# Performance work log

Measured on AMD Instinct MI355X. Metric: run time of the kernel, lower is better.

Reference implementation:

```python
import jax, jax.numpy as jnp
import numpy as np
from jax import lax

B, PN, NS = 8, 16384, 256
KDIM, HID = 512, 384
HALF = HID // 2
EPS = 1e-5


def setup_inputs() -> dict:
    key = jax.random.key(0)
    ks = jax.random.split(key, 12)
    s = lambda fan: np.float32(1.0 / np.sqrt(fan))
    inp = {
        "p": jax.random.normal(ks[0], (B, PN, 3), jnp.float32),
        "N": NS,
        "patch_feature": jax.random.normal(ks[1], (B, KDIM, 1), jnp.float32),
        # Linear(k_dim, hidden)
        "W_feat": jax.random.normal(ks[2], (KDIM, HID), jnp.float32) * s(KDIM),
        "b_feat": jax.random.normal(ks[3], (HID,), jnp.float32) * s(KDIM),
        # Linear(3, hidden//2)
        "W_coord": jax.random.normal(ks[4], (3, HALF), jnp.float32) * s(3),
        "b_coord": jax.random.normal(ks[5], (HALF,), jnp.float32) * s(3),
        # Conv1d(hidden+hidden//2, hidden, 1) == per-point linear, weight (out,in)
        "W1": jax.random.normal(ks[6], (HID, HID + HALF), jnp.float32) * s(HID + HALF),
        "b1": jax.random.normal(ks[7], (HID,), jnp.float32) * s(HID + HALF),
        "g1": jnp.ones((HID,), jnp.float32),
        "be1": jnp.zeros((HID,), jnp.float32),
        # Conv1d(hidden, hidden, 1)
        "W2": jax.random.normal(ks[8], (HID, HID), jnp.float32) * s(HID),
        "b2": jax.random.normal(ks[9], (HID,), jnp.float32) * s(HID),
        "g2": jnp.ones((HID,), jnp.float32),
        "be2": jnp.zeros((HID,), jnp.float32),
    }
    return inp


def farthest_point_sample(points, k):
    """points: (B, N, C) -> (B, k, C). Deterministic start index 0 per batch."""
    b, n, c = points.shape

    def step(carry, _):
        dist, far = carry
        centroid = jnp.take_along_axis(points, far[:, None, None], axis=1)  # (B,1,C)
        d = jnp.sum((points - centroid) ** 2, axis=-1)                      # (B,N)
        dist = jnp.minimum(dist, d)
        new_far = jnp.argmax(dist, axis=-1)
        return (dist, new_far), far

    init = (jnp.full((b, n), 1e10, points.dtype), jnp.zeros((b,), jnp.int32))
    _, idx = lax.scan(step, init, None, length=k)  # idx: (k, B)
    idx = idx.T                                    # (B, k)
    return jnp.take_along_axis(points, idx[:, :, None], axis=1)  # (B,k,C)


def batchnorm(x, gamma, beta):
    """x: (B, L, C); training-mode BN over (B, L) per channel (biased var)."""
    mean = jnp.mean(x, axis=(0, 1))
    var = jnp.var(x, axis=(0, 1))
    return (x - mean) * lax.rsqrt(var + EPS) * gamma + beta


def reference(p, N, patch_feature, W_feat, b_feat, W_coord, b_coord,
              W1, b1, g1, be1, W2, b2, g2, be2):
    b, pn, _ = p.shape
    global_feat = patch_feature[..., 0] @ W_feat + b_feat          # (B, HID)
    global_feat = jnp.broadcast_to(global_feat[:, None, :], (b, N, HID))
    local_feat = p @ W_coord + b_coord                              # (B, PN, HALF)
    if N != pn:
        local_feat = farthest_point_sample(local_feat, N)           # (B, N, HALF)
    combined = jnp.concatenate([global_feat, local_feat], axis=-1)  # (B, N, HID+HALF)
    h = jnp.einsum("bnc,oc->bno", combined, W1) + b1
    h = jax.nn.relu(batchnorm(h, g1, be1))
    h = jnp.einsum("bnc,oc->bno", h, W2) + b2
    h = jax.nn.relu(batchnorm(h, g2, be2))
    return h  # (B, N, HID)
```

## Files before the change

kernel.cpp:

```cpp
#include <hip/hip_runtime.h>

#define BATCH 8
#define PN    16384
#define NSAMP 256
#define KDIM  512
#define HID   384
#define HALF  192
#define CIN   576
#define ROWS  2048
#define BN_EPS 1e-5f

#define OFF_GF   0
#define OFF_W1T  3072
#define OFF_GFW  76800
#define OFF_W2T  224256
#define OFF_IDX  371712
#define OFF_H1   373760
#define OFF_H2   1160192
#define OFF_SUM1 1946624
#define OFF_SQ1  1947008
#define OFF_SUM2 1947392
#define OFF_SQ2  1947776

typedef float v2f __attribute__((ext_vector_type(2)));

#define DPP_MAX(v, ctrl)                                                   \
  v = fmaxf(v, __int_as_float(__builtin_amdgcn_update_dpp(                 \
          0, __float_as_int(v), (ctrl), 0xf, 0xf, true)))

__global__ __launch_bounds__(1024)
void k_main(const float* p, const float* Wc,
            const float* pf, const float* Wf,
            const float* bfe, const float* W1,
            const float* b1v, const float* W2,
            float* ws) {
  __shared__ float s[KDIM];
  __shared__ float Msh[6];
  __shared__ unsigned gb[2];
  __shared__ int widx[2];
  int blk = blockIdx.x, t = threadIdx.x;

  if (blk >= 8) {
    if (blk < 16) {
      for (int sI = (blk - 8) * 1024 + t; sI < HID * HALF; sI += 8192) {
        int o = sI / HALF, c = sI % HALF;
        ws[OFF_W1T + c * HID + o] = W1[o * CIN + HID + c];
      }
    } else if (blk < 24) {
      for (int sI = (blk - 16) * 1024 + t; sI < HID * HID; sI += 8192) {
        int o = sI / HID, c = sI % HID;
        ws[OFF_W2T + c * HID + o] = W2[sI];
      }
    } else if (blk < 32) {
      int b = blk - 24;
      if (t < KDIM) s[t] = pf[b * KDIM + t];
      __syncthreads();
      float acc = 0.f;
      if (t < HID) {
        acc = bfe[t];
        for (int k = 0; k < KDIM; k++) acc = fmaf(s[k], Wf[k * HID + t], acc);
        ws[OFF_GF + b * HID + t] = acc;
      }
      __syncthreads();
      if (t < HID) s[t] = acc;
      __syncthreads();
      if (t < HID) {
        float g = b1v[t];
        const float* w1row = W1 + t * CIN;
        for (int c = 0; c < HID; c++) g = fmaf(s[c], w1row[c], g);
        ws[OFF_GFW + b * HID + t] = g;
      }
    } else {
      for (int i = t; i < 1536; i += 1024) ws[OFF_SUM1 + i] = 0.f;
    }
    return;
  }

  int b = blk;
  int* idx_out = (int*)(ws + OFF_IDX);

  if (t < 64) {
    double g0 = 0, g1 = 0, g2 = 0, g3 = 0, g4 = 0, g5 = 0;
    for (int k = t; k < HALF; k += 64) {
      double w0 = (double)Wc[k];
      double w1 = (double)Wc[HALF + k];
      double w2 = (double)Wc[2 * HALF + k];
      g0 += w0 * w0; g1 += w0 * w1; g2 += w0 * w2;
      g3 += w1 * w1; g4 += w1 * w2; g5 += w2 * w2;
    }
    for (int off = 32; off; off >>= 1) {
      g0 += __shfl_down(g0, off, 64); g1 += __shfl_down(g1, off, 64);
      g2 += __shfl_down(g2, off, 64); g3 += __shfl_down(g3, off, 64);
      g4 += __shfl_down(g4, off, 64); g5 += __shfl_down(g5, off, 64);
    }
    if (t == 0) {
      double l00 = sqrt(g0);
      double l10 = g1 / l00, l20 = g2 / l00;
      double l11 = sqrt(g3 - l10 * l10);
      double l21 = (g4 - l10 * l20) / l11;
      double l22 = sqrt(g5 - l20 * l20 - l21 * l21);
      Msh[0] = (float)l00; Msh[1] = (float)l10; Msh[2] = (float)l20;
      Msh[3] = (float)l11; Msh[4] = (float)l21; Msh[5] = (float)l22;
    }
  }
  __syncthreads();
  float m00 = Msh[0], m10 = Msh[1], m20 = Msh[2];
  float m11 = Msh[3], m21 = Msh[4], m22 = Msh[5];

  const float* pb = p + b * PN * 3;
  float4* qws = (float4*)(ws + OFF_H1) + b * PN;
  v2f qx[8], qy[8], qz[8], nq[8], dist[8];
#pragma unroll
  for (int j = 0; j < 8; j++) {
    int i0 = ((2 * j) << 10) + t;
    int i1 = i0 + 1024;
    float x0 = pb[i0 * 3], y0 = pb[i0 * 3 + 1], z0 = pb[i0 * 3 + 2];
    float x1 = pb[i1 * 3], y1 = pb[i1 * 3 + 1], z1 = pb[i1 * 3 + 2];
    qx[j] = (v2f){fmaf(m00, x0, fmaf(m10, y0, m20 * z0)),
                  fmaf(m00, x1, fmaf(m10, y1, m20 * z1))};
    qy[j] = (v2f){fmaf(m11, y0, m21 * z0), fmaf(m11, y1, m21 * z1)};
    qz[j] = (v2f){m22 * z0, m22 * z1};
    nq[j] = __builtin_elementwise_fma(
        qx[j], qx[j],
        __builtin_elementwise_fma(qy[j], qy[j], qz[j] * qz[j]));
    dist[j] = (v2f){1e10f, 1e10f};
    qws[i0] = make_float4(qx[j].x, qy[j].x, qz[j].x, nq[j].x);
    qws[i1] = make_float4(qx[j].y, qy[j].y, qz[j].y, nq[j].y);
  }

  if (t == 0) {
    widx[0] = 0x7fffffff; widx[1] = 0x7fffffff;
    gb[0] = 0u; gb[1] = 0u;
  }
  __syncthreads();

  int far = 0;
  int par = 0;
  for (int k = 0; k < NSAMP; k++) {
    float4 qc = qws[far];
    float cx2 = -2.f * qc.x, cy2 = -2.f * qc.y, cz2 = -2.f * qc.z;
    v2f cxv = (v2f){cx2, cx2}, cyv = (v2f){cy2, cy2}, czv = (v2f){cz2, cz2};
    v2f ncv = (v2f){qc.w, qc.w};
#pragma unroll
    for (int j = 0; j < 8; j++) {
      v2f base = nq[j] + ncv;
      v2f d = __builtin_elementwise_fma(
          qx[j], cxv,
          __builtin_elementwise_fma(qy[j], cyv,
              __builtin_elementwise_fma(qz[j], czv, base)));
      dist[j] = __builtin_elementwise_min(dist[j], d);
    }
    if (t == 0) {
      idx_out[b * NSAMP + k] = far;
      widx[par] = 0x7fffffff;
      gb[par ^ 1] = 0u;
    }
    v2f t0v = __builtin_elementwise_max(dist[0], dist[1]);
    v2f t1v = __builtin_elementwise_max(dist[2], dist[3]);
    v2f t2v = __builtin_elementwise_max(dist[4], dist[5]);
    v2f t3v = __builtin_elementwise_max(dist[6], dist[7]);
    t0v = __builtin_elementwise_max(t0v, t1v);
    t2v = __builtin_elementwise_max(t2v, t3v);
    t0v = __builtin_elementwise_max(t0v, t2v);
    float tmax = fmaxf(t0v.x, t0v.y);
    float wv = tmax;
    DPP_MAX(wv, 0x111);
    DPP_MAX(wv, 0x112);
    DPP_MAX(wv, 0x114);
    DPP_MAX(wv, 0x118);
    DPP_MAX(wv, 0x142);
    DPP_MAX(wv, 0x143);
    if ((t & 63) == 63)
      atomicMax(&gb[par], __float_as_uint(fmaxf(wv, 0.f)));
    __syncthreads();
    float gmax = __uint_as_float(gb[par]);
    if (tmax == gmax) {
      int mi = 0x7fffffff;
#pragma unroll
      for (int j = 7; j >= 0; j--) {
        int i0 = ((2 * j) << 10) + t;
        mi = (dist[j].y == gmax) ? i0 + 1024 : mi;
        mi = (dist[j].x == gmax) ? i0 : mi;
      }
      atomicMin(&widx[par], mi);
    }
    __syncthreads();
    far = widx[par];
    par ^= 1;
  }
}

__global__ __launch_bounds__(384) void k_gemm1(const float* p,
                                               const float* Wc,
                                               const float* bc,
                                               float* ws) {
  __shared__ __align__(16) float ct[HALF * 8];
  int t = threadIdx.x;
  int row0 = blockIdx.x * 8;
  int b = row0 >> 8;
  const int* fidx = (const int*)(ws + OFF_IDX);
  for (int sI = t; sI < 8 * HALF; sI += 384) {
    int r = sI / HALF, co = sI % HALF;
    int row = row0 + r;
    int i = fidx[row];
    const float* pp = p + (b * PN + i) * 3;
    float val = bc[co];
    val = fmaf(pp[0], Wc[co], val);
    val = fmaf(pp[1], Wc[HALF + co], val);
    val = fmaf(pp[2], Wc[2 * HALF + co], val);
    ct[co * 8 + r] = val;
  }
  __syncthreads();
  const float* w1t = ws + OFF_W1T;
  float acc[8] = {0.f, 0.f, 0.f, 0.f, 0.f, 0.f, 0.f, 0.f};
  for (int c = 0; c < HALF; c++) {
    float w = w1t[c * HID + t];
    float4 a0 = *(const float4*)(ct + c * 8);
    float4 a1 = *(const float4*)(ct + c * 8 + 4);
    acc[0] = fmaf(a0.x, w, acc[0]); acc[1] = fmaf(a0.y, w, acc[1]);
    acc[2] = fmaf(a0.z, w, acc[2]); acc[3] = fmaf(a0.w, w, acc[3]);
    acc[4] = fmaf(a1.x, w, acc[4]); acc[5] = fmaf(a1.y, w, acc[5]);
    acc[6] = fmaf(a1.z, w, acc[6]); acc[7] = fmaf(a1.w, w, acc[7]);
  }
  float base = ws[OFF_GFW + b * HID + t];
  float sv = 0.f, sq = 0.f;
#pragma unroll
  for (int r = 0; r < 8; r++) {
    float v = acc[r] + base;
    ws[OFF_H1 + (row0 + r) * HID + t] = v;
    sv += v; sq = fmaf(v, v, sq);
  }
  atomicAdd(&ws[OFF_SUM1 + t], sv);
  atomicAdd(&ws[OFF_SQ1 + t], sq);
}

__global__ __launch_bounds__(384) void k_gemm2(const float* b2,
                                               const float* g1,
                                               const float* be1,
                                               float* ws) {
  __shared__ __align__(16) float ht[HID * 8];
  __shared__ float sc1s[HID], sh1s[HID];
  int t = threadIdx.x;
  int row0 = blockIdx.x * 8;
  {
    float m = ws[OFF_SUM1 + t] * (1.f / ROWS);
    float v = ws[OFF_SQ1 + t] * (1.f / ROWS) - m * m;
    float inv = 1.f / sqrtf(v + BN_EPS);
    float sc = inv * g1[t];
    sc1s[t] = sc;
    sh1s[t] = be1[t] - m * sc;
  }
  __syncthreads();
  for (int sI = t; sI < 8 * HID; sI += 384) {
    int r = sI / HID, c = sI % HID;
    float x = fmaf(ws[OFF_H1 + (row0 + r) * HID + c], sc1s[c], sh1s[c]);
    ht[c * 8 + r] = fmaxf(x, 0.f);
  }
  __syncthreads();
  const float* w2t = ws + OFF_W2T;
  float acc[8] = {0.f, 0.f, 0.f, 0.f, 0.f, 0.f, 0.f, 0.f};
  for (int c = 0; c < HID; c++) {
    float w = w2t[c * HID + t];
    float4 a0 = *(const float4*)(ht + c * 8);
    float4 a1 = *(const float4*)(ht + c * 8 + 4);
    acc[0] = fmaf(a0.x, w, acc[0]); acc[1] = fmaf(a0.y, w, acc[1]);
    acc[2] = fmaf(a0.z, w, acc[2]); acc[3] = fmaf(a0.w, w, acc[3]);
    acc[4] = fmaf(a1.x, w, acc[4]); acc[5] = fmaf(a1.y, w, acc[5]);
    acc[6] = fmaf(a1.z, w, acc[6]); acc[7] = fmaf(a1.w, w, acc[7]);
  }
  float bias = b2[t];
  float sv = 0.f, sq = 0.f;
#pragma unroll
  for (int r = 0; r < 8; r++) {
    float v = acc[r] + bias;
    ws[OFF_H2 + (row0 + r) * HID + t] = v;
    sv += v; sq = fmaf(v, v, sq);
  }
  atomicAdd(&ws[OFF_SUM2 + t], sv);
  atomicAdd(&ws[OFF_SQ2 + t], sq);
}

__global__ __launch_bounds__(256) void k_out(const float* ws, const float* g2,
                                             const float* be2, float* out) {
  int gid = blockIdx.x * 256 + threadIdx.x;
  int i = gid * 4;
  int c = i % HID;
  float4 h  = *(const float4*)(ws + OFF_H2 + i);
  float4 s2 = *(const float4*)(ws + OFF_SUM2 + c);
  float4 q2 = *(const float4*)(ws + OFF_SQ2 + c);
  float4 gv = *(const float4*)(g2 + c);
  float4 bv = *(const float4*)(be2 + c);
  float4 r;
#define BN2(comp) {                                                  \
    float m  = s2.comp * (1.f / ROWS);                               \
    float v  = q2.comp * (1.f / ROWS) - m * m;                       \
    float sc = (1.f / sqrtf(v + BN_EPS)) * gv.comp;                  \
    float sh = bv.comp - m * sc;                                     \
    r.comp = fmaxf(fmaf(h.comp, sc, sh), 0.f); }
  BN2(x) BN2(y) BN2(z) BN2(w)
#undef BN2
  ((float4*)out)[gid] = r;
}

extern "C" void kernel_launch(void* const* d_in, const int* in_sizes, int n_in,
                              void* d_out, int out_size, void* d_ws, size_t ws_size,
                              hipStream_t stream) {
  const float* p   = (const float*)d_in[0];
  const float* pf  = (const float*)d_in[2];
  const float* Wf  = (const float*)d_in[3];
  const float* bfe = (const float*)d_in[4];
  const float* Wc  = (const float*)d_in[5];
  const float* bc  = (const float*)d_in[6];
  const float* W1  = (const float*)d_in[7];
  const float* b1  = (const float*)d_in[8];
  const float* g1  = (const float*)d_in[9];
  const float* be1 = (const float*)d_in[10];
  const float* W2  = (const float*)d_in[11];
  const float* b2  = (const float*)d_in[12];
  const float* g2  = (const float*)d_in[13];
  const float* be2 = (const float*)d_in[14];
  float* ws = (float*)d_ws;

  hipLaunchKernelGGL(k_main,  dim3(33),  dim3(1024), 0, stream,
                     p, Wc, pf, Wf, bfe, W1, b1, W2, ws);
  hipLaunchKernelGGL(k_gemm1, dim3(256), dim3(384), 0, stream, p, Wc, bc, ws);
  hipLaunchKernelGGL(k_gemm2, dim3(256), dim3(384), 0, stream, b2, g1, be1, ws);
  hipLaunchKernelGGL(k_out,   dim3(768), dim3(256), 0, stream,
                     ws, g2, be2, (float*)d_out);
}
```

Measured before the change: 495.9 us.

## Fuse FPS argmax into single packed 64-bit atomicMax per iteration

Each wave now finds its own argmax index with a DPP reduction on the inverted index, then packs the max distance and inverted index into a 64-bit key for one shared atomicMax. This removes the second barrier and the atomicMin pass from every farthest-point-sampling iteration, and a three-slot rotating buffer replaces the double-buffered reset. Each iteration costs more per-wave DPP work and 64-bit LDS atomics in exchange for one fewer block-wide synchronisation.

```diff
diff --git a/kernel.cpp b/kernel.cpp
--- a/kernel.cpp
+++ b/kernel.cpp
@@ -27,6 +27,12 @@
 #define DPP_MAX(v, ctrl)                                                   \
   v = fmaxf(v, __int_as_float(__builtin_amdgcn_update_dpp(                 \
           0, __float_as_int(v), (ctrl), 0xf, 0xf, true)))
+#define DPP_UMAX(v, ctrl)                                                  \
+  {                                                                        \
+    unsigned _o = (unsigned)__builtin_amdgcn_update_dpp(                   \
+        0, (int)(v), (ctrl), 0xf, 0xf, true);                              \
+    v = (_o > (v)) ? _o : (v);                                             \
+  }
 
 __global__ __launch_bounds__(1024)
 void k_main(const float* p, const float* Wc,
@@ -36,8 +42,7 @@
             float* ws) {
   __shared__ float s[KDIM];
   __shared__ float Msh[6];
-  __shared__ unsigned gb[2];
-  __shared__ int widx[2];
+  __shared__ unsigned long long gkey[3];
   int blk = blockIdx.x, t = threadIdx.x;
 
   if (blk >= 8) {
@@ -128,14 +133,10 @@
     qws[i1] = make_float4(qx[j].y, qy[j].y, qz[j].y, nq[j].y);
   }
 
-  if (t == 0) {
-    widx[0] = 0x7fffffff; widx[1] = 0x7fffffff;
-    gb[0] = 0u; gb[1] = 0u;
-  }
+  if (t == 0) { gkey[0] = 0ull; gkey[1] = 0ull; gkey[2] = 0ull; }
   __syncthreads();
 
   int far = 0;
-  int par = 0;
   for (int k = 0; k < NSAMP; k++) {
     float4 qc = qws[far];
     float cx2 = -2.f * qc.x, cy2 = -2.f * qc.y, cz2 = -2.f * qc.z;
@@ -150,11 +151,7 @@
               __builtin_elementwise_fma(qz[j], czv, base)));
       dist[j] = __builtin_elementwise_min(dist[j], d);
     }
-    if (t == 0) {
-      idx_out[b * NSAMP + k] = far;
-      widx[par] = 0x7fffffff;
-      gb[par ^ 1] = 0u;
-    }
+    if (t == 0) idx_out[b * NSAMP + k] = far;
     v2f t0v = __builtin_elementwise_max(dist[0], dist[1]);
     v2f t1v = __builtin_elementwise_max(dist[2], dist[3]);
     v2f t2v = __builtin_elementwise_max(dist[4], dist[5]);
@@ -163,6 +160,13 @@
     t2v = __builtin_elementwise_max(t2v, t3v);
     t0v = __builtin_elementwise_max(t0v, t2v);
     float tmax = fmaxf(t0v.x, t0v.y);
+    int mi = 0x7fffffff;
+#pragma unroll
+    for (int j = 7; j >= 0; j--) {
+      int i0 = ((2 * j) << 10) + t;
+      mi = (dist[j].y == tmax) ? i0 + 1024 : mi;
+      mi = (dist[j].x == tmax) ? i0 : mi;
+    }
     float wv = tmax;
     DPP_MAX(wv, 0x111);
     DPP_MAX(wv, 0x112);
@@ -170,23 +174,25 @@
     DPP_MAX(wv, 0x118);
     DPP_MAX(wv, 0x142);
     DPP_MAX(wv, 0x143);
-    if ((t & 63) == 63)
-      atomicMax(&gb[par], __float_as_uint(fmaxf(wv, 0.f)));
+    float swv = __int_as_float(
+        __builtin_amdgcn_readlane(__float_as_int(wv), 63));
+    unsigned umi = (tmax == swv) ? ~(unsigned)mi : 0u;
+    DPP_UMAX(umi, 0x111);
+    DPP_UMAX(umi, 0x112);
+    DPP_UMAX(umi, 0x114);
+    DPP_UMAX(umi, 0x118);
+    DPP_UMAX(umi, 0x142);
+    DPP_UMAX(umi, 0x143);
+    if ((t & 63) == 63) {
+      unsigned long long key =
+          ((unsigned long long)__float_as_uint(fmaxf(swv, 0.f)) << 32) |
+          (unsigned long long)umi;
+      atomicMax(&gkey[k % 3], key);
+    }
     __syncthreads();
-    float gmax = __uint_as_float(gb[par]);
-    if (tmax == gmax) {
-      int mi = 0x7fffffff;
-#pragma unroll
-      for (int j = 7; j >= 0; j--) {
-        int i0 = ((2 * j) << 10) + t;
-        mi = (dist[j].y == gmax) ? i0 + 1024 : mi;
-        mi = (dist[j].x == gmax) ? i0 : mi;
-      }
-      atomicMin(&widx[par], mi);
-    }
-    __syncthreads();
-    far = widx[par];
-    par ^= 1;
+    unsigned long long bk = gkey[k % 3];
+    if (t == 0) gkey[(k + 2) % 3] = 0ull;
+    far = (int)(~(unsigned)bk);
   }
 }
 
```

New measurement: 527.5 us. +6.4%, slower.
